# Kernel tuning notes

Hardware: AMD Instinct MI355X
Metric: run time of the kernel (lower is better)

## Reference

```python
import jax, jax.numpy as jnp
import numpy as np

B, S, IN, OUT = 64, 512, 256, 256   # batch, seq_len, in/out features
R, NB, E = 40, 3, 262144            # num_rels, num_bases, num_edges
N = B * S                           # total nodes in batched graph


def setup_inputs() -> dict:
    key = jax.random.key(0)
    ks = jax.random.split(key, 6)
    text = jax.random.normal(ks[0], (B, S, IN), jnp.float32)
    src = jax.random.randint(ks[1], (E,), 0, N)
    dst = jax.random.randint(ks[2], (E,), 0, N)
    rel = jax.random.randint(ks[3], (E,), 0, R)
    bases = jax.random.normal(ks[4], (NB, IN, OUT), jnp.float32) / np.sqrt(IN).astype(np.float32)
    comp = jax.random.normal(ks[5], (R, NB), jnp.float32)
    bias = jnp.zeros((OUT,), jnp.float32)
    return dict(text=text, src=src, dst=dst, rel=rel, bases=bases, comp=comp, bias=bias)


def reference(text, src, dst, rel, bases, comp, bias):
    Bt, St, INt = text.shape
    h = text.reshape(-1, INt)                       # [N, in] flattened node feats
    n_nodes = h.shape[0]
    # project every node through every basis once: [N, num_bases, out]
    t = jnp.einsum('ni,bio->nbo', h, bases)
    # per-edge message: sum_b comp[rel_e, b] * (h_src @ basis_b)  -> [E, out]
    msg = jnp.einsum('eb,ebo->eo', comp[rel], t[src])
    # scatter-sum aggregation to destination nodes
    agg = jax.ops.segment_sum(msg, dst, num_segments=n_nodes)   # [N, out]
    out = jax.nn.relu(agg + bias)
    return out.reshape(Bt, -1, out.shape[-1])
```

## Files before the change

kernel.cpp:

```cpp
#include <hip/hip_runtime.h>
#include <cstdint>

#define N_NODES 32768
#define IN_F    256
#define OUT_F   256
#define NBASES  3
#define N_EDGES 262144
#define K_DIM   (NBASES * IN_F)
#define ZROWS   32

typedef __attribute__((ext_vector_type(8))) short bf16x8;
typedef __attribute__((ext_vector_type(4))) float f32x4;

__device__ __forceinline__ unsigned short f2bf(float x) {
    union { float f; unsigned int u; } c; c.f = x;
    unsigned int u = c.u;
    u = (u + 0x7FFFu + ((u >> 16) & 1u)) >> 16;
    return (unsigned short)u;
}
__device__ __forceinline__ float bf2f(unsigned short h) {
    union { unsigned int u; float f; } c; c.u = ((unsigned int)h) << 16;
    return c.f;
}

__device__ __forceinline__ void async_copy16(const void* g, void* l) {
    __builtin_amdgcn_global_load_lds(
        (const __attribute__((address_space(1))) unsigned int*)g,
        (__attribute__((address_space(3))) unsigned int*)l, 16, 0, 0);
}

__global__ __launch_bounds__(256) void prep_kernel(
    const float* __restrict__ text,
    const float* __restrict__ bases,
    unsigned short* __restrict__ hb,
    unsigned short* __restrict__ Wt,
    int* __restrict__ counts)
{
    const int tid = threadIdx.x;
    if (blockIdx.x < 8192) {
        int i = blockIdx.x * 256 + tid;
        float4 v = reinterpret_cast<const float4*>(text)[i];
        ushort4 o;
        o.x = f2bf(v.x); o.y = f2bf(v.y); o.z = f2bf(v.z); o.w = f2bf(v.w);
        reinterpret_cast<ushort4*>(hb)[i] = o;
    } else if (blockIdx.x < 8384) {
        int tb = blockIdx.x - 8192;
        int kb = tb % 24, ob = tb / 24;
        __shared__ float tile[32][33];
        int c = tid & 31, r8 = tid >> 5;
        #pragma unroll
        for (int i = 0; i < 4; ++i) {
            int r = r8 + 8 * i;
            tile[r][c] = bases[(size_t)(kb * 32 + r) * OUT_F + ob * 32 + c];
        }
        __syncthreads();
        #pragma unroll
        for (int i = 0; i < 4; ++i) {
            int r = r8 + 8 * i;
            Wt[(size_t)(ob * 32 + r) * K_DIM + kb * 32 + c] = f2bf(tile[c][r]);
        }
    } else {
        int i = (blockIdx.x - 8384) * 256 + tid;
        counts[i] = 0;
    }
}

__global__ __launch_bounds__(256) void hist_kernel(
    const int* __restrict__ dst, int* __restrict__ counts)
{
    int e4 = blockIdx.x * 256 + threadIdx.x;
    int4 d = reinterpret_cast<const int4*>(dst)[e4];
    atomicAdd(&counts[d.x], 1);
    atomicAdd(&counts[d.y], 1);
    atomicAdd(&counts[d.z], 1);
    atomicAdd(&counts[d.w], 1);
}

__global__ __launch_bounds__(1024) void scan_kernel(
    int* __restrict__ counts,
    int* __restrict__ offsets)
{
    __shared__ int wsum[16];
    const int tid = threadIdx.x;
    const int wave = tid >> 6, lane = tid & 63;
    const int base = tid * 32;
    int local[32];
    int sum = 0;
    #pragma unroll
    for (int k8 = 0; k8 < 8; ++k8) {
        int4 v = reinterpret_cast<const int4*>(counts + base)[k8];
        local[k8 * 4 + 0] = v.x; local[k8 * 4 + 1] = v.y;
        local[k8 * 4 + 2] = v.z; local[k8 * 4 + 3] = v.w;
        sum += v.x + v.y + v.z + v.w;
    }
    int inc = sum;
    #pragma unroll
    for (int off = 1; off < 64; off <<= 1) {
        int v = __shfl_up(inc, off);
        if (lane >= off) inc += v;
    }
    if (lane == 63) wsum[wave] = inc;
    __syncthreads();
    if (wave == 0 && lane < 16) {
        int v = wsum[lane];
        #pragma unroll
        for (int off = 1; off < 16; off <<= 1) {
            int u = __shfl_up(v, off);
            if (lane >= off) v += u;
        }
        wsum[lane] = v;
    }
    __syncthreads();
    int run = inc - sum + (wave ? wsum[wave - 1] : 0);
    #pragma unroll
    for (int k = 0; k < 32; ++k) {
        offsets[base + k] = run;
        counts[base + k] = run;
        run += local[k];
    }
    if (tid == 1023) offsets[N_NODES] = run;
}

__global__ __launch_bounds__(256) void scatter_kernel(
    const int* __restrict__ dst, const int* __restrict__ src,
    const int* __restrict__ rel, const float* __restrict__ comp,
    int* __restrict__ cursor, int2* __restrict__ packed2)
{
    int e4 = blockIdx.x * 256 + threadIdx.x;
    int4 d = reinterpret_cast<const int4*>(dst)[e4];
    int4 s = reinterpret_cast<const int4*>(src)[e4];
    int4 r = reinterpret_cast<const int4*>(rel)[e4];
    int dd[4] = { d.x, d.y, d.z, d.w };
    int ss[4] = { s.x, s.y, s.z, s.w };
    int rr[4] = { r.x, r.y, r.z, r.w };
    #pragma unroll
    for (int q = 0; q < 4; ++q) {
        float c0 = comp[rr[q] * 3 + 0];
        float c1 = comp[rr[q] * 3 + 1];
        float c2 = comp[rr[q] * 3 + 2];
        int w0 = ss[q] | ((int)f2bf(c0) << 16);
        int w1 = (int)f2bf(c1) | ((int)f2bf(c2) << 16);
        int pos = atomicAdd(&cursor[dd[q]], 1);
        packed2[pos] = make_int2(w0, w1);
    }
}

__global__ __launch_bounds__(256, 2) void fused_kernel(
    const unsigned short* __restrict__ hb,
    const int2* __restrict__ packed2,
    const int* __restrict__ offsets,
    const unsigned short* __restrict__ Wt,
    const float* __restrict__ bias,
    float* __restrict__ out)
{
    __shared__ __align__(16) unsigned short Zs[ZROWS * 96 * 8];
    __shared__ __align__(16) unsigned short Bs[256 * 4 * 8];

    const int tid  = threadIdx.x;
    const int wave = tid >> 6, lane = tid & 63;
    const int quad = lane >> 4, l16 = lane & 15;
    const int m0 = blockIdx.x * ZROWS;

    for (int i = 0; i < 8; ++i) {
        const int m = wave * 8 + i;
        const int node = m0 + m;
        const int start = offsets[node];
        const int end   = offsets[node + 1];

        float a[12] = {};
        for (int cb = start; cb < end; cb += 64) {
            int idx = cb + lane;
            int wx = 0, wy = 0;
            if (idx < end) { int2 w = packed2[idx]; wx = w.x; wy = w.y; }
            int cnt = min(64, end - cb);
            for (int j = 0; j < cnt; j += 4) {
                float c0[4], c1[4], c2[4];
                ushort4 u[4];
                #pragma unroll
                for (int q = 0; q < 4; ++q) {
                    int p0 = __shfl(wx, j + q);
                    int p1 = __shfl(wy, j + q);
                    int s = p0 & 0xFFFF;
                    c0[q] = bf2f((unsigned short)((unsigned)p0 >> 16));
                    c1[q] = bf2f((unsigned short)(p1 & 0xFFFF));
                    c2[q] = bf2f((unsigned short)((unsigned)p1 >> 16));
                    u[q] = *reinterpret_cast<const ushort4*>(
                        hb + (size_t)s * IN_F + lane * 4);
                }
                #pragma unroll
                for (int q = 0; q < 4; ++q) {
                    float v[4] = { bf2f(u[q].x), bf2f(u[q].y),
                                   bf2f(u[q].z), bf2f(u[q].w) };
                    #pragma unroll
                    for (int k = 0; k < 4; ++k) {
                        a[k]     += c0[q] * v[k];
                        a[4 + k] += c1[q] * v[k];
                        a[8 + k] += c2[q] * v[k];
                    }
                }
            }
        }

        #pragma unroll
        for (int seg = 0; seg < 3; ++seg) {
            int oct  = seg * 32 + (lane >> 1);
            int phys = oct ^ (m & 7);
            ushort4 o;
            o.x = f2bf(a[seg * 4 + 0]); o.y = f2bf(a[seg * 4 + 1]);
            o.z = f2bf(a[seg * 4 + 2]); o.w = f2bf(a[seg * 4 + 3]);
            *reinterpret_cast<ushort4*>(
                &Zs[(m * 96 + phys) * 8 + (lane & 1) * 4]) = o;
        }
    }
    __syncthreads();

    const unsigned short* gB[4];
    int lB[4];
    #pragma unroll
    for (int c = 0; c < 4; ++c) {
        int p = c * 256 + wave * 64 + lane;
        int col = p >> 2;
        int logical = (p & 3) ^ ((col >> 1) & 3);
        gB[c] = Wt + (size_t)col * K_DIM + logical * 8;
        lB[c] = (c * 256 + wave * 64) * 8;
    }

    f32x4 acc[2][4] = {};
    for (int s = 0; s < 24; ++s) {
        __syncthreads();
        #pragma unroll
        for (int c = 0; c < 4; ++c)
            async_copy16(gB[c] + s * 32, &Bs[lB[c]]);
        __syncthreads();

        bf16x8 af[2], bfr[4];
        #pragma unroll
        for (int i = 0; i < 2; ++i) {
            int m = i * 16 + l16;
            int phys = (s * 4 + quad) ^ (m & 7);
            af[i] = *reinterpret_cast<const bf16x8*>(&Zs[(m * 96 + phys) * 8]);
        }
        #pragma unroll
        for (int j = 0; j < 4; ++j) {
            int col = wave * 64 + j * 16 + l16;
            int physo = quad ^ ((col >> 1) & 3);
            bfr[j] = *reinterpret_cast<const bf16x8*>(&Bs[(col * 4 + physo) * 8]);
        }
        #pragma unroll
        for (int i = 0; i < 2; ++i)
            #pragma unroll
            for (int j = 0; j < 4; ++j)
                acc[i][j] = __builtin_amdgcn_mfma_f32_16x16x32_bf16(
                    af[i], bfr[j], acc[i][j], 0, 0, 0);
    }

    #pragma unroll
    for (int j = 0; j < 4; ++j) {
        int col = wave * 64 + j * 16 + l16;
        float bv = bias[col];
        #pragma unroll
        for (int i = 0; i < 2; ++i) {
            int row_base = m0 + i * 16 + quad * 4;
            #pragma unroll
            for (int r = 0; r < 4; ++r)
                out[(size_t)(row_base + r) * OUT_F + col] =
                    fmaxf(acc[i][j][r] + bv, 0.f);
        }
    }
}

extern "C" void kernel_launch(void* const* d_in, const int* in_sizes, int n_in,
                              void* d_out, int out_size, void* d_ws, size_t ws_size,
                              hipStream_t stream) {
    const float* text  = (const float*)d_in[0];
    const int*   src   = (const int*)d_in[1];
    const int*   dst   = (const int*)d_in[2];
    const int*   rel   = (const int*)d_in[3];
    const float* bases = (const float*)d_in[4];
    const float* comp  = (const float*)d_in[5];
    const float* bias  = (const float*)d_in[6];
    float* out = (float*)d_out;

    char* p = (char*)d_ws;
    unsigned short* hb = (unsigned short*)p;      p += (size_t)N_NODES * IN_F * 2;
    int2* packed2 = (int2*)p;                     p += (size_t)N_EDGES * 8;
    int* offsets  = (int*)p;                      p += (size_t)(N_NODES + 4) * 4;
    int* counts   = (int*)p;                      p += (size_t)N_NODES * 4;
    unsigned short* Wt = (unsigned short*)p;

    prep_kernel<<<8512, 256, 0, stream>>>(text, bases, hb, Wt, counts);
    hist_kernel<<<N_EDGES / 1024, 256, 0, stream>>>(dst, counts);
    scan_kernel<<<1, 1024, 0, stream>>>(counts, offsets);
    scatter_kernel<<<N_EDGES / 1024, 256, 0, stream>>>(
        dst, src, rel, comp, counts, packed2);
    fused_kernel<<<N_NODES / ZROWS, 256, 0, stream>>>(
        hb, packed2, offsets, Wt, bias, out);
}
```

Before: 212.0 us.

## Split fused gather-GEMM into two K-halves to halve LDS and raise occupancy

The fused kernel now processes the input feature dimension in two halves of 128. For each half it gathers and aggregates neighbor features into a smaller shared Z tile, then runs the matching 12 MFMA K-steps. Each half-wave handles alternate edges with 4 features per lane, and the two halves are combined with a cross-lane xor shuffle. This halves the Z LDS footprint, so launch bounds rise to 4 blocks per CU for more latency hiding on the irregular gathers. The cost is an extra shuffle reduction, more barriers, and a second pass over each node's edge list and packed metadata.

```diff
diff --git a/kernel.cpp b/kernel.cpp
--- a/kernel.cpp
+++ b/kernel.cpp
@@ -145,7 +145,7 @@
     }
 }
 
-__global__ __launch_bounds__(256, 2) void fused_kernel(
+__global__ __launch_bounds__(256, 4) void fused_kernel(
     const unsigned short* __restrict__ hb,
     const int2* __restrict__ packed2,
     const int* __restrict__ offsets,
@@ -153,66 +153,15 @@
     const float* __restrict__ bias,
     float* __restrict__ out)
 {
-    __shared__ __align__(16) unsigned short Zs[ZROWS * 96 * 8];
+    __shared__ __align__(16) unsigned short Zs[ZROWS * 48 * 8];
     __shared__ __align__(16) unsigned short Bs[256 * 4 * 8];
 
     const int tid  = threadIdx.x;
     const int wave = tid >> 6, lane = tid & 63;
     const int quad = lane >> 4, l16 = lane & 15;
+    const int half = lane >> 5;
+    const int f4   = lane & 31;
     const int m0 = blockIdx.x * ZROWS;
-
-    for (int i = 0; i < 8; ++i) {
-        const int m = wave * 8 + i;
-        const int node = m0 + m;
-        const int start = offsets[node];
-        const int end   = offsets[node + 1];
-
-        float a[12] = {};
-        for (int cb = start; cb < end; cb += 64) {
-            int idx = cb + lane;
-            int wx = 0, wy = 0;
-            if (idx < end) { int2 w = packed2[idx]; wx = w.x; wy = w.y; }
-            int cnt = min(64, end - cb);
-            for (int j = 0; j < cnt; j += 4) {
-                float c0[4], c1[4], c2[4];
-                ushort4 u[4];
-                #pragma unroll
-                for (int q = 0; q < 4; ++q) {
-                    int p0 = __shfl(wx, j + q);
-                    int p1 = __shfl(wy, j + q);
-                    int s = p0 & 0xFFFF;
-                    c0[q] = bf2f((unsigned short)((unsigned)p0 >> 16));
-                    c1[q] = bf2f((unsigned short)(p1 & 0xFFFF));
-                    c2[q] = bf2f((unsigned short)((unsigned)p1 >> 16));
-                    u[q] = *reinterpret_cast<const ushort4*>(
-                        hb + (size_t)s * IN_F + lane * 4);
-                }
-                #pragma unroll
-                for (int q = 0; q < 4; ++q) {
-                    float v[4] = { bf2f(u[q].x), bf2f(u[q].y),
-                                   bf2f(u[q].z), bf2f(u[q].w) };
-                    #pragma unroll
-                    for (int k = 0; k < 4; ++k) {
-                        a[k]     += c0[q] * v[k];
-                        a[4 + k] += c1[q] * v[k];
-                        a[8 + k] += c2[q] * v[k];
-                    }
-                }
-            }
-        }
-
-        #pragma unroll
-        for (int seg = 0; seg < 3; ++seg) {
-            int oct  = seg * 32 + (lane >> 1);
-            int phys = oct ^ (m & 7);
-            ushort4 o;
-            o.x = f2bf(a[seg * 4 + 0]); o.y = f2bf(a[seg * 4 + 1]);
-            o.z = f2bf(a[seg * 4 + 2]); o.w = f2bf(a[seg * 4 + 3]);
-            *reinterpret_cast<ushort4*>(
-                &Zs[(m * 96 + phys) * 8 + (lane & 1) * 4]) = o;
-        }
-    }
-    __syncthreads();
 
     const unsigned short* gB[4];
     int lB[4];
@@ -226,32 +175,98 @@
     }
 
     f32x4 acc[2][4] = {};
-    for (int s = 0; s < 24; ++s) {
+
+    for (int t = 0; t < 2; ++t) {
         __syncthreads();
-        #pragma unroll
-        for (int c = 0; c < 4; ++c)
-            async_copy16(gB[c] + s * 32, &Bs[lB[c]]);
+
+        const unsigned short* hbase = hb + t * 128 + f4 * 4;
+        for (int i = 0; i < 8; ++i) {
+            const int m = wave * 8 + i;
+            const int node = m0 + m;
+            const int start = offsets[node];
+            const int end   = offsets[node + 1];
+
+            float a[12] = {};
+            for (int cb = start; cb < end; cb += 64) {
+                int idx = cb + lane;
+                int wx = 0, wy = 0;
+                if (idx < end) { int2 w = packed2[idx]; wx = w.x; wy = w.y; }
+                int cnt = min(64, end - cb);
+                for (int j = 0; j < cnt; j += 8) {
+                    float c0[4], c1[4], c2[4];
+                    ushort4 u[4];
+                    #pragma unroll
+                    for (int q = 0; q < 4; ++q) {
+                        int e = j + 2 * q + half;
+                        int p0 = __shfl(wx, e);
+                        int p1 = __shfl(wy, e);
+                        int s = p0 & 0xFFFF;
+                        c0[q] = bf2f((unsigned short)((unsigned)p0 >> 16));
+                        c1[q] = bf2f((unsigned short)(p1 & 0xFFFF));
+                        c2[q] = bf2f((unsigned short)((unsigned)p1 >> 16));
+                        u[q] = *reinterpret_cast<const ushort4*>(
+                            hbase + (size_t)s * IN_F);
+                    }
+                    #pragma unroll
+                    for (int q = 0; q < 4; ++q) {
+                        float v[4] = { bf2f(u[q].x), bf2f(u[q].y),
+                                       bf2f(u[q].z), bf2f(u[q].w) };
+                        #pragma unroll
+                        for (int k = 0; k < 4; ++k) {
+                            a[k]     += c0[q] * v[k];
+                            a[4 + k] += c1[q] * v[k];
+                            a[8 + k] += c2[q] * v[k];
+                        }
+                    }
+                }
+            }
+            #pragma unroll
+            for (int k = 0; k < 12; ++k) a[k] += __shfl_xor(a[k], 32);
+            if (half == 0) {
+                #pragma unroll
+                for (int seg = 0; seg < 3; ++seg) {
+                    int oct  = seg * 16 + (f4 >> 1);
+                    int phys = oct ^ (m & 7);
+                    ushort4 o;
+                    o.x = f2bf(a[seg * 4 + 0]); o.y = f2bf(a[seg * 4 + 1]);
+                    o.z = f2bf(a[seg * 4 + 2]); o.w = f2bf(a[seg * 4 + 3]);
+                    *reinterpret_cast<ushort4*>(
+                        &Zs[(m * 48 + phys) * 8 + (f4 & 1) * 4]) = o;
+                }
+            }
+        }
         __syncthreads();
 
-        bf16x8 af[2], bfr[4];
-        #pragma unroll
-        for (int i = 0; i < 2; ++i) {
-            int m = i * 16 + l16;
-            int phys = (s * 4 + quad) ^ (m & 7);
-            af[i] = *reinterpret_cast<const bf16x8*>(&Zs[(m * 96 + phys) * 8]);
-        }
-        #pragma unroll
-        for (int j = 0; j < 4; ++j) {
-            int col = wave * 64 + j * 16 + l16;
-            int physo = quad ^ ((col >> 1) & 3);
-            bfr[j] = *reinterpret_cast<const bf16x8*>(&Bs[(col * 4 + physo) * 8]);
-        }
-        #pragma unroll
-        for (int i = 0; i < 2; ++i)
-            #pragma unroll
-            for (int j = 0; j < 4; ++j)
-                acc[i][j] = __builtin_amdgcn_mfma_f32_16x16x32_bf16(
-                    af[i], bfr[j], acc[i][j], 0, 0, 0);
+        for (int s = 0; s < 12; ++s) {
+            if (s) __syncthreads();
+            int kbase = (s >> 2) * 256 + t * 128 + (s & 3) * 32;
+            #pragma unroll
+            for (int c = 0; c < 4; ++c)
+                async_copy16(gB[c] + kbase, &Bs[lB[c]]);
+            __syncthreads();
+
+            bf16x8 af[2], bfr[4];
+            #pragma unroll
+            for (int i = 0; i < 2; ++i) {
+                int m = i * 16 + l16;
+                int phys = (s * 4 + quad) ^ (m & 7);
+                af[i] = *reinterpret_cast<const bf16x8*>(
+                    &Zs[(m * 48 + phys) * 8]);
+            }
+            #pragma unroll
+            for (int j = 0; j < 4; ++j) {
+                int col = wave * 64 + j * 16 + l16;
+                int physo = quad ^ ((col >> 1) & 3);
+                bfr[j] = *reinterpret_cast<const bf16x8*>(
+                    &Bs[(col * 4 + physo) * 8]);
+            }
+            #pragma unroll
+            for (int i = 0; i < 2; ++i)
+                #pragma unroll
+                for (int j = 0; j < 4; ++j)
+                    acc[i][j] = __builtin_amdgcn_mfma_f32_16x16x32_bf16(
+                        af[i], bfr[j], acc[i][j], 0, 0, 0);
+        }
     }
 
     #pragma unroll
```

Result: faster. 203.9 us (-3.8%).

## Split fused aggregate+GEMM into separate aggregation and tiled double-buffered GEMM kernels

Applied to the files above, without the earlier changes.

Replaces the fused kernel, which gathered 32 node rows into LDS and then ran a small GEMM, with two kernels. The first is a one-wave-per-node aggregation that writes the combined basis features Z to global memory. The second is a 128x128-tile GEMM that double-buffers its A and B tiles in LDS. The aim is better occupancy and load balance for the gather phase and more operand reuse in the GEMM, at the cost of an extra 48MB round trip for Z through global memory plus one more launch.

```diff
diff --git a/kernel.cpp b/kernel.cpp
--- a/kernel.cpp
+++ b/kernel.cpp
@@ -7,7 +7,6 @@
 #define NBASES  3
 #define N_EDGES 262144
 #define K_DIM   (NBASES * IN_F)
-#define ZROWS   32
 
 typedef __attribute__((ext_vector_type(8))) short bf16x8;
 typedef __attribute__((ext_vector_type(4))) float f32x4;
@@ -145,122 +144,136 @@
     }
 }
 
-__global__ __launch_bounds__(256, 2) void fused_kernel(
+__global__ __launch_bounds__(256) void agg_kernel(
     const unsigned short* __restrict__ hb,
     const int2* __restrict__ packed2,
     const int* __restrict__ offsets,
-    const unsigned short* __restrict__ Wt,
+    unsigned short* __restrict__ z)
+{
+    const int node = blockIdx.x * 4 + (threadIdx.x >> 6);
+    const int lane = threadIdx.x & 63;
+    const int start = offsets[node];
+    const int end   = offsets[node + 1];
+
+    float a0[4] = {}, a1[4] = {}, a2[4] = {};
+    const unsigned short* hp = hb + lane * 4;
+
+    for (int cb = start; cb < end; cb += 64) {
+        int idx = cb + lane;
+        int wx = 0, wy = 0;
+        if (idx < end) { int2 w = packed2[idx]; wx = w.x; wy = w.y; }
+        int cnt = min(64, end - cb);
+        for (int j = 0; j < cnt; j += 8) {
+            float c0[8], c1[8], c2[8];
+            ushort4 u[8];
+            #pragma unroll
+            for (int q = 0; q < 8; ++q) {
+                int p0 = __shfl(wx, j + q);
+                int p1 = __shfl(wy, j + q);
+                int s = p0 & 0xFFFF;
+                float m = (j + q < cnt) ? 1.f : 0.f;
+                c0[q] = m * bf2f((unsigned short)((unsigned)p0 >> 16));
+                c1[q] = m * bf2f((unsigned short)(p1 & 0xFFFF));
+                c2[q] = m * bf2f((unsigned short)((unsigned)p1 >> 16));
+                u[q] = *reinterpret_cast<const ushort4*>(hp + (size_t)s * IN_F);
+            }
+            #pragma unroll
+            for (int q = 0; q < 8; ++q) {
+                float v[4] = { bf2f(u[q].x), bf2f(u[q].y),
+                               bf2f(u[q].z), bf2f(u[q].w) };
+                #pragma unroll
+                for (int k = 0; k < 4; ++k) {
+                    a0[k] += c0[q] * v[k];
+                    a1[k] += c1[q] * v[k];
+                    a2[k] += c2[q] * v[k];
+                }
+            }
+        }
+    }
+
+    unsigned short* zp = z + (size_t)node * K_DIM + lane * 4;
+    ushort4 o;
+    o.x = f2bf(a0[0]); o.y = f2bf(a0[1]); o.z = f2bf(a0[2]); o.w = f2bf(a0[3]);
+    *reinterpret_cast<ushort4*>(zp) = o;
+    o.x = f2bf(a1[0]); o.y = f2bf(a1[1]); o.z = f2bf(a1[2]); o.w = f2bf(a1[3]);
+    *reinterpret_cast<ushort4*>(zp + 256) = o;
+    o.x = f2bf(a2[0]); o.y = f2bf(a2[1]); o.z = f2bf(a2[2]); o.w = f2bf(a2[3]);
+    *reinterpret_cast<ushort4*>(zp + 512) = o;
+}
+
+__global__ __launch_bounds__(256) void gemm_kernel(
+    const unsigned short* __restrict__ A,
+    const unsigned short* __restrict__ Bt,
     const float* __restrict__ bias,
     float* __restrict__ out)
 {
-    __shared__ __align__(16) unsigned short Zs[ZROWS * 96 * 8];
-    __shared__ __align__(16) unsigned short Bs[256 * 4 * 8];
+    __shared__ __align__(16) unsigned short As[2][128 * 32];
+    __shared__ __align__(16) unsigned short Bs[2][128 * 32];
 
     const int tid  = threadIdx.x;
     const int wave = tid >> 6, lane = tid & 63;
     const int quad = lane >> 4, l16 = lane & 15;
-    const int m0 = blockIdx.x * ZROWS;
-
-    for (int i = 0; i < 8; ++i) {
-        const int m = wave * 8 + i;
-        const int node = m0 + m;
-        const int start = offsets[node];
-        const int end   = offsets[node + 1];
-
-        float a[12] = {};
-        for (int cb = start; cb < end; cb += 64) {
-            int idx = cb + lane;
-            int wx = 0, wy = 0;
-            if (idx < end) { int2 w = packed2[idx]; wx = w.x; wy = w.y; }
-            int cnt = min(64, end - cb);
-            for (int j = 0; j < cnt; j += 4) {
-                float c0[4], c1[4], c2[4];
-                ushort4 u[4];
-                #pragma unroll
-                for (int q = 0; q < 4; ++q) {
-                    int p0 = __shfl(wx, j + q);
-                    int p1 = __shfl(wy, j + q);
-                    int s = p0 & 0xFFFF;
-                    c0[q] = bf2f((unsigned short)((unsigned)p0 >> 16));
-                    c1[q] = bf2f((unsigned short)(p1 & 0xFFFF));
-                    c2[q] = bf2f((unsigned short)((unsigned)p1 >> 16));
-                    u[q] = *reinterpret_cast<const ushort4*>(
-                        hb + (size_t)s * IN_F + lane * 4);
-                }
-                #pragma unroll
-                for (int q = 0; q < 4; ++q) {
-                    float v[4] = { bf2f(u[q].x), bf2f(u[q].y),
-                                   bf2f(u[q].z), bf2f(u[q].w) };
-                    #pragma unroll
-                    for (int k = 0; k < 4; ++k) {
-                        a[k]     += c0[q] * v[k];
-                        a[4 + k] += c1[q] * v[k];
-                        a[8 + k] += c2[q] * v[k];
-                    }
-                }
+    const int wm = (wave & 1) * 64, wn = (wave >> 1) * 64;
+    const int m0 = blockIdx.x * 128, n0 = blockIdx.y * 128;
+
+    f32x4 acc[4][4] = {};
+
+    const unsigned short *ga[2], *gb[2];
+    int lab[2];
+    #pragma unroll
+    for (int c = 0; c < 2; ++c) {
+        int p = c * 256 + wave * 64 + lane;
+        int row = p >> 2;
+        int oct = (p & 3) ^ ((row >> 1) & 3);
+        ga[c] = A  + (size_t)(m0 + row) * K_DIM + oct * 8;
+        gb[c] = Bt + (size_t)(n0 + row) * K_DIM + oct * 8;
+        lab[c] = (c * 256 + wave * 64) * 8;
+    }
+
+    #pragma unroll
+    for (int c = 0; c < 2; ++c) {
+        async_copy16(ga[c], &As[0][lab[c]]);
+        async_copy16(gb[c], &Bs[0][lab[c]]);
+    }
+
+    int cur = 0;
+    for (int step = 0; step < K_DIM / 32; ++step) {
+        __syncthreads();
+        int k1 = (step + 1) * 32;
+        if (k1 < K_DIM) {
+            #pragma unroll
+            for (int c = 0; c < 2; ++c) {
+                async_copy16(ga[c] + k1, &As[cur ^ 1][lab[c]]);
+                async_copy16(gb[c] + k1, &Bs[cur ^ 1][lab[c]]);
             }
         }
 
-        #pragma unroll
-        for (int seg = 0; seg < 3; ++seg) {
-            int oct  = seg * 32 + (lane >> 1);
-            int phys = oct ^ (m & 7);
-            ushort4 o;
-            o.x = f2bf(a[seg * 4 + 0]); o.y = f2bf(a[seg * 4 + 1]);
-            o.z = f2bf(a[seg * 4 + 2]); o.w = f2bf(a[seg * 4 + 3]);
-            *reinterpret_cast<ushort4*>(
-                &Zs[(m * 96 + phys) * 8 + (lane & 1) * 4]) = o;
-        }
-    }
-    __syncthreads();
-
-    const unsigned short* gB[4];
-    int lB[4];
-    #pragma unroll
-    for (int c = 0; c < 4; ++c) {
-        int p = c * 256 + wave * 64 + lane;
-        int col = p >> 2;
-        int logical = (p & 3) ^ ((col >> 1) & 3);
-        gB[c] = Wt + (size_t)col * K_DIM + logical * 8;
-        lB[c] = (c * 256 + wave * 64) * 8;
-    }
-
-    f32x4 acc[2][4] = {};
-    for (int s = 0; s < 24; ++s) {
-        __syncthreads();
-        #pragma unroll
-        for (int c = 0; c < 4; ++c)
-            async_copy16(gB[c] + s * 32, &Bs[lB[c]]);
-        __syncthreads();
-
-        bf16x8 af[2], bfr[4];
-        #pragma unroll
-        for (int i = 0; i < 2; ++i) {
-            int m = i * 16 + l16;
-            int phys = (s * 4 + quad) ^ (m & 7);
-            af[i] = *reinterpret_cast<const bf16x8*>(&Zs[(m * 96 + phys) * 8]);
-        }
-        #pragma unroll
-        for (int j = 0; j < 4; ++j) {
-            int col = wave * 64 + j * 16 + l16;
-            int physo = quad ^ ((col >> 1) & 3);
-            bfr[j] = *reinterpret_cast<const bf16x8*>(&Bs[(col * 4 + physo) * 8]);
-        }
-        #pragma unroll
-        for (int i = 0; i < 2; ++i)
+        bf16x8 af[4], bfr[4];
+        #pragma unroll
+        for (int i = 0; i < 4; ++i) {
+            int row = wm + i * 16 + l16;
+            int oph = quad ^ ((row >> 1) & 3);
+            af[i] = *reinterpret_cast<const bf16x8*>(&As[cur][(row * 4 + oph) * 8]);
+            int nn   = wn + i * 16 + l16;
+            int oph2 = quad ^ ((nn >> 1) & 3);
+            bfr[i] = *reinterpret_cast<const bf16x8*>(&Bs[cur][(nn * 4 + oph2) * 8]);
+        }
+        #pragma unroll
+        for (int i = 0; i < 4; ++i)
             #pragma unroll
             for (int j = 0; j < 4; ++j)
                 acc[i][j] = __builtin_amdgcn_mfma_f32_16x16x32_bf16(
                     af[i], bfr[j], acc[i][j], 0, 0, 0);
+        cur ^= 1;
     }
 
     #pragma unroll
     for (int j = 0; j < 4; ++j) {
-        int col = wave * 64 + j * 16 + l16;
+        int col = n0 + wn + j * 16 + l16;
         float bv = bias[col];
         #pragma unroll
-        for (int i = 0; i < 2; ++i) {
-            int row_base = m0 + i * 16 + quad * 4;
+        for (int i = 0; i < 4; ++i) {
+            int row_base = m0 + wm + i * 16 + quad * 4;
             #pragma unroll
             for (int r = 0; r < 4; ++r)
                 out[(size_t)(row_base + r) * OUT_F + col] =
@@ -282,6 +295,7 @@
     float* out = (float*)d_out;
 
     char* p = (char*)d_ws;
+    unsigned short* z  = (unsigned short*)p;      p += (size_t)N_NODES * K_DIM * 2;
     unsigned short* hb = (unsigned short*)p;      p += (size_t)N_NODES * IN_F * 2;
     int2* packed2 = (int2*)p;                     p += (size_t)N_EDGES * 8;
     int* offsets  = (int*)p;                      p += (size_t)(N_NODES + 4) * 4;
@@ -293,6 +307,7 @@
     scan_kernel<<<1, 1024, 0, stream>>>(counts, offsets);
     scatter_kernel<<<N_EDGES / 1024, 256, 0, stream>>>(
         dst, src, rel, comp, counts, packed2);
-    fused_kernel<<<N_NODES / ZROWS, 256, 0, stream>>>(
-        hb, packed2, offsets, Wt, bias, out);
-}
+    agg_kernel<<<N_NODES / 4, 256, 0, stream>>>(hb, packed2, offsets, z);
+    gemm_kernel<<<dim3(N_NODES / 128, OUT_F / 128), 256, 0, stream>>>(
+        z, Wt, bias, out);
+}
```

Result: faster. 185.0 us (-12.8%).
